# Optimization experiments

Measured on AMD Instinct MI355X. Metric: run time of the kernel, lower is better.

Reference implementation:

```python
import jax, jax.numpy as jnp
import numpy as np
from jax.scipy.special import logsumexp

B, S, T = 512, 512, 64


def setup_inputs() -> dict:
    key = jax.random.key(0)
    k1, k2, k3, k4, k5 = jax.random.split(key, 5)
    inputs = jax.random.normal(k1, (B, S, T), dtype=jnp.float32)
    tags = jax.random.randint(k2, (B, S), 0, T, dtype=jnp.int64)
    mask = jnp.ones((B, S), dtype=bool)
    # xavier_normal for (T, T): std = sqrt(2 / (T + T))
    transitions = jax.random.normal(k3, (T, T), dtype=jnp.float32) * np.sqrt(2.0 / (T + T))
    start_transitions = jax.random.normal(k4, (T,), dtype=jnp.float32)
    end_transitions = jax.random.normal(k5, (T,), dtype=jnp.float32)
    return {"inputs": inputs, "tags": tags, "mask": mask,
            "transitions": transitions,
            "start_transitions": start_transitions,
            "end_transitions": end_transitions}


def _input_likelihood(logits, mask, transitions, start_transitions, end_transitions):
    # logits: (B,S,T) -> time-major (S,B,T)
    logits_t = jnp.swapaxes(logits, 0, 1)
    mask_t = jnp.swapaxes(mask, 0, 1)
    alpha0 = start_transitions[None, :] + logits_t[0]  # (B,T)

    def step(alpha, xs):
        logit_i, m_i = xs  # (B,T), (B,)
        # inner[b, prev, cur] = alpha[b,prev] + logit_i[b,cur] + transitions[prev,cur]
        inner = alpha[:, :, None] + logit_i[:, None, :] + transitions[None, :, :]
        new_alpha = logsumexp(inner, axis=1)
        alpha = jnp.where(m_i[:, None], new_alpha, alpha)
        return alpha, None

    alpha, _ = jax.lax.scan(step, alpha0, (logits_t[1:], mask_t[1:]))
    stops = alpha + end_transitions[None, :]
    return logsumexp(stops, axis=-1)  # (B,)


def _joint_likelihood(logits, tags, mask, transitions, start_transitions, end_transitions):
    maskf = mask.astype(logits.dtype)  # (B,S)
    score = start_transitions[tags[:, 0]]  # (B,)
    # transition scores for steps 0..S-2 -> 1..S-1, masked by mask[:,1:]
    trans = transitions[tags[:, :-1], tags[:, 1:]] * maskf[:, 1:]
    # emission scores for steps 0..S-2, masked by mask[:,:-1]
    emit = jnp.take_along_axis(logits[:, :-1, :], tags[:, :-1, None], axis=2)[..., 0] * maskf[:, :-1]
    score = score + trans.sum(axis=1) + emit.sum(axis=1)
    last_idx = maskf.sum(axis=1).astype(jnp.int32) - 1
    last_tags = jnp.take_along_axis(tags, last_idx[:, None].astype(tags.dtype), axis=1)[:, 0]
    last_input_score = jnp.take_along_axis(logits[:, -1, :], last_tags[:, None], axis=1)[:, 0]
    score = score + end_transitions[last_tags] + last_input_score * maskf[:, -1]
    return score  # (B,)


def reference(inputs, tags, mask, transitions, start_transitions, end_transitions):
    log_denominator = _input_likelihood(inputs, mask, transitions, start_transitions, end_transitions)
    log_numerator = _joint_likelihood(inputs, tags, mask, transitions, start_transitions, end_transitions)
    return jnp.sum(log_numerator - log_denominator)
```

## Files before the change

kernel.cpp:

```cpp
#include <hip/hip_runtime.h>

#define CRF_B 512
#define CRF_S 512
#define CRF_T 64

__global__ __launch_bounds__(64, 1) void crf_fused_kernel(
    const float* __restrict__ logits,
    const int*   __restrict__ tags_raw,
    const float* __restrict__ trans,
    const float* __restrict__ start_t,
    const float* __restrict__ end_t,
    float* __restrict__ out)
{
    const int b = blockIdx.x;
    const int j = threadIdx.x;

    bool is64 = true;
    #pragma unroll
    for (int w = 1; w < 64; w += 2) is64 = is64 && (tags_raw[w] == 0);

    const float* lb = logits + (size_t)b * CRF_S * CRF_T;
    const int tbase = b * CRF_S;

    float num = 0.f;
    #pragma unroll
    for (int kk = 0; kk < CRF_S / 64; ++kk) {
        int i = kk * 64 + j;
        int ti = is64 ? tags_raw[(size_t)(tbase + i) * 2] : tags_raw[tbase + i];
        num += lb[i * CRF_T + ti];
        if (i == 0) {
            num += start_t[ti];
        } else {
            int tp = is64 ? tags_raw[(size_t)(tbase + i - 1) * 2]
                          : tags_raw[tbase + i - 1];
            num += trans[tp * CRF_T + ti];
        }
        if (i == CRF_S - 1) num += end_t[ti];
    }
    #pragma unroll
    for (int m = 32; m >= 1; m >>= 1) num += __shfl_xor(num, m, 64);

    float et[CRF_T];
    #pragma unroll
    for (int t = 0; t < CRF_T; ++t) et[t] = __expf(trans[t * CRF_T + j]);

    float a = __expf(start_t[j] + lb[j]);
    int K = 0;
    float elog = __expf(lb[CRF_T + j]);
    float lg_next = lb[2 * CRF_T + j];

    #pragma unroll 2
    for (int i = 1; i < CRF_S; ++i) {
        unsigned mbits = (unsigned)__builtin_amdgcn_readfirstlane(__float_as_int(a));
        int k = (int)(mbits >> 23) - 127;
        K += k;
        float scale = __int_as_float((unsigned)(127 - k) << 23);
        float mult = elog * scale;

        float acc0 = 0.f, acc1 = 0.f, acc2 = 0.f, acc3 = 0.f;
        int ai = __float_as_int(a);
        #pragma unroll
        for (int t = 0; t < CRF_T; t += 4) {
            acc0 = fmaf(__int_as_float(__builtin_amdgcn_readlane(ai, t + 0)), et[t + 0], acc0);
            acc1 = fmaf(__int_as_float(__builtin_amdgcn_readlane(ai, t + 1)), et[t + 1], acc1);
            acc2 = fmaf(__int_as_float(__builtin_amdgcn_readlane(ai, t + 2)), et[t + 2], acc2);
            acc3 = fmaf(__int_as_float(__builtin_amdgcn_readlane(ai, t + 3)), et[t + 3], acc3);
        }
        float s = (acc0 + acc1) + (acc2 + acc3);
        a = s * mult;

        elog = __expf(lg_next);
        int nxt = (i + 2 < CRF_S) ? (i + 2) : (CRF_S - 1);
        lg_next = lb[nxt * CRF_T + j];
    }

    float v = a * __expf(end_t[j]);
    #pragma unroll
    for (int m = 32; m >= 1; m >>= 1) v += __shfl_xor(v, m, 64);

    if (j == 0) {
        float logZ = __logf(v) + (float)K * 0.69314718055994531f;
        atomicAdd(out, num - logZ);
    }
}

extern "C" void kernel_launch(void* const* d_in, const int* in_sizes, int n_in,
                              void* d_out, int out_size, void* d_ws, size_t ws_size,
                              hipStream_t stream) {
    const float* logits  = (const float*)d_in[0];
    const int*   tags    = (const int*)d_in[1];
    const float* trans   = (const float*)d_in[3];
    const float* start_t = (const float*)d_in[4];
    const float* end_t   = (const float*)d_in[5];
    float* out = (float*)d_out;

    hipMemsetAsync(out, 0, sizeof(float) * (size_t)out_size, stream);
    crf_fused_kernel<<<dim3(CRF_B), dim3(64), 0, stream>>>(
        logits, tags, trans, start_t, end_t, out);
}
```

Measured before the change: 213.1 us.

## Broadcast alpha through LDS and use packed FMA for forward recursion

Replaces the 64 per-step readlane broadcasts of the alpha vector with one LDS store followed by float4 broadcast reads. The matvec now accumulates with v_pk_fma_f32 into eight packed accumulators. The aim is to remove the serialized scalar readlane path and halve the FMA instruction count. In exchange each step adds LDS store-to-load latency, relies on wave barriers for ordering, and drops the unroll-by-2 of the sequential loop.

```diff
diff --git a/kernel.cpp b/kernel.cpp
--- a/kernel.cpp
+++ b/kernel.cpp
@@ -3,6 +3,10 @@
 #define CRF_B 512
 #define CRF_S 512
 #define CRF_T 64
+
+typedef float v2f __attribute__((ext_vector_type(2)));
+
+#define PKFMA(acc, x, y) asm("v_pk_fma_f32 %0, %1, %2, %0" : "+v"(acc) : "v"(x), "v"(y))
 
 __global__ __launch_bounds__(64, 1) void crf_fused_kernel(
     const float* __restrict__ logits,
@@ -14,6 +18,8 @@
 {
     const int b = blockIdx.x;
     const int j = threadIdx.x;
+
+    __shared__ __align__(16) float a_lds[CRF_T];
 
     bool is64 = true;
     #pragma unroll
@@ -40,34 +46,50 @@
     #pragma unroll
     for (int m = 32; m >= 1; m >>= 1) num += __shfl_xor(num, m, 64);
 
-    float et[CRF_T];
+    v2f et2[CRF_T / 2];
     #pragma unroll
-    for (int t = 0; t < CRF_T; ++t) et[t] = __expf(trans[t * CRF_T + j]);
+    for (int t = 0; t < CRF_T; t += 2) {
+        et2[t / 2].x = __expf(trans[(t + 0) * CRF_T + j]);
+        et2[t / 2].y = __expf(trans[(t + 1) * CRF_T + j]);
+    }
 
     float a = __expf(start_t[j] + lb[j]);
     int K = 0;
     float elog = __expf(lb[CRF_T + j]);
     float lg_next = lb[2 * CRF_T + j];
 
-    #pragma unroll 2
     for (int i = 1; i < CRF_S; ++i) {
+        a_lds[j] = a;
+        __builtin_amdgcn_wave_barrier();
+
         unsigned mbits = (unsigned)__builtin_amdgcn_readfirstlane(__float_as_int(a));
         int k = (int)(mbits >> 23) - 127;
         K += k;
         float scale = __int_as_float((unsigned)(127 - k) << 23);
         float mult = elog * scale;
 
-        float acc0 = 0.f, acc1 = 0.f, acc2 = 0.f, acc3 = 0.f;
-        int ai = __float_as_int(a);
+        v2f p0 = {0.f, 0.f}, p1 = {0.f, 0.f}, p2 = {0.f, 0.f}, p3 = {0.f, 0.f};
+        v2f p4 = {0.f, 0.f}, p5 = {0.f, 0.f}, p6 = {0.f, 0.f}, p7 = {0.f, 0.f};
         #pragma unroll
-        for (int t = 0; t < CRF_T; t += 4) {
-            acc0 = fmaf(__int_as_float(__builtin_amdgcn_readlane(ai, t + 0)), et[t + 0], acc0);
-            acc1 = fmaf(__int_as_float(__builtin_amdgcn_readlane(ai, t + 1)), et[t + 1], acc1);
-            acc2 = fmaf(__int_as_float(__builtin_amdgcn_readlane(ai, t + 2)), et[t + 2], acc2);
-            acc3 = fmaf(__int_as_float(__builtin_amdgcn_readlane(ai, t + 3)), et[t + 3], acc3);
+        for (int t = 0; t < CRF_T; t += 16) {
+            float4 av0 = *(const float4*)&a_lds[t + 0];
+            float4 av1 = *(const float4*)&a_lds[t + 4];
+            float4 av2 = *(const float4*)&a_lds[t + 8];
+            float4 av3 = *(const float4*)&a_lds[t + 12];
+            v2f x;
+            x.x = av0.x; x.y = av0.y; PKFMA(p0, x, et2[(t >> 1) + 0]);
+            x.x = av0.z; x.y = av0.w; PKFMA(p1, x, et2[(t >> 1) + 1]);
+            x.x = av1.x; x.y = av1.y; PKFMA(p2, x, et2[(t >> 1) + 2]);
+            x.x = av1.z; x.y = av1.w; PKFMA(p3, x, et2[(t >> 1) + 3]);
+            x.x = av2.x; x.y = av2.y; PKFMA(p4, x, et2[(t >> 1) + 4]);
+            x.x = av2.z; x.y = av2.w; PKFMA(p5, x, et2[(t >> 1) + 5]);
+            x.x = av3.x; x.y = av3.y; PKFMA(p6, x, et2[(t >> 1) + 6]);
+            x.x = av3.z; x.y = av3.w; PKFMA(p7, x, et2[(t >> 1) + 7]);
         }
-        float s = (acc0 + acc1) + (acc2 + acc3);
-        a = s * mult;
+        __builtin_amdgcn_wave_barrier();
+
+        v2f r = ((p0 + p1) + (p2 + p3)) + ((p4 + p5) + (p6 + p7));
+        a = (r.x + r.y) * mult;
 
         elog = __expf(lg_next);
         int nxt = (i + 2 < CRF_S) ? (i + 2) : (CRF_S - 1);
```

Measured after the change: 294.8 us. 1.38x slower.

## Compute CRF forward recurrence with bf16 MFMA instead of readlane FMAs

Applied to the files above, without the earlier changes.

Replaces the per-step 64-element readlane/FMA dot product with bf16 MFMA 16x16x32 instructions. The exp(transitions) matrix is held in MFMA A fragments and the alpha vector is re-packed into B fragments each step. Rescaling moves to the exponent of the next step's emission, which is prefetched two steps ahead. This targets the serial readlane latency in the recurrence, at the cost of bf16 rounding of alpha and transitions that could exceed tolerance over 512 steps.

```diff
diff --git a/kernel.cpp b/kernel.cpp
--- a/kernel.cpp
+++ b/kernel.cpp
@@ -1,8 +1,21 @@
 #include <hip/hip_runtime.h>
+#include <hip/hip_bf16.h>
+#include <string.h>
 
 #define CRF_B 512
 #define CRF_S 512
 #define CRF_T 64
+#define LOG2E 1.4426950408889634f
+#define LN2   0.69314718055994531f
+
+typedef float  f32x4  __attribute__((ext_vector_type(4)));
+typedef short  bf16x8 __attribute__((ext_vector_type(8)));
+union Frag { bf16x8 f; unsigned d[4]; };
+
+__device__ __forceinline__ unsigned pack2(float lo, float hi) {
+    __hip_bfloat162 h2 = __float22bfloat162_rn(make_float2(lo, hi));
+    unsigned u; memcpy(&u, &h2, 4); return u;
+}
 
 __global__ __launch_bounds__(64, 1) void crf_fused_kernel(
     const float* __restrict__ logits,
@@ -12,20 +25,20 @@
     const float* __restrict__ end_t,
     float* __restrict__ out)
 {
-    const int b = blockIdx.x;
-    const int j = threadIdx.x;
+    const int b   = blockIdx.x;
+    const int L   = threadIdx.x;
+    const int Q   = L >> 4;
+    const int n16 = L & 15;
+    const float* lb = logits + (size_t)b * CRF_S * CRF_T;
 
     bool is64 = true;
     #pragma unroll
     for (int w = 1; w < 64; w += 2) is64 = is64 && (tags_raw[w] == 0);
-
-    const float* lb = logits + (size_t)b * CRF_S * CRF_T;
     const int tbase = b * CRF_S;
-
     float num = 0.f;
     #pragma unroll
     for (int kk = 0; kk < CRF_S / 64; ++kk) {
-        int i = kk * 64 + j;
+        int i = kk * 64 + L;
         int ti = is64 ? tags_raw[(size_t)(tbase + i) * 2] : tags_raw[tbase + i];
         num += lb[i * CRF_T + ti];
         if (i == 0) {
@@ -40,48 +53,103 @@
     #pragma unroll
     for (int m = 32; m >= 1; m >>= 1) num += __shfl_xor(num, m, 64);
 
-    float et[CRF_T];
+    Frag AF[4][2];
     #pragma unroll
-    for (int t = 0; t < CRF_T; ++t) et[t] = __expf(trans[t * CRF_T + j]);
+    for (int m = 0; m < 4; ++m)
+        #pragma unroll
+        for (int c = 0; c < 2; ++c) {
+            float v[8];
+            #pragma unroll
+            for (int u = 0; u < 8; ++u) {
+                int row = 16 * ((u >> 2) + 2 * c) + 4 * Q + (u & 3);
+                v[u] = __expf(trans[row * CRF_T + 16 * m + n16]);
+            }
+            #pragma unroll
+            for (int h = 0; h < 4; ++h)
+                AF[m][c].d[h] = pack2(v[2 * h], v[2 * h + 1]);
+        }
 
-    float a = __expf(start_t[j] + lb[j]);
-    int K = 0;
-    float elog = __expf(lb[CRF_T + j]);
-    float lg_next = lb[2 * CRF_T + j];
+    f32x4 a0[4];
+    #pragma unroll
+    for (int mm = 0; mm < 4; ++mm) {
+        f32x4 lg = *(const f32x4*)(lb + 16 * mm + 4 * Q);
+        f32x4 st = *(const f32x4*)(start_t + 16 * mm + 4 * Q);
+        #pragma unroll
+        for (int e = 0; e < 4; ++e) a0[mm][e] = __expf(st[e] + lg[e]);
+    }
+    Frag BF[2];
+    #pragma unroll
+    for (int c = 0; c < 2; ++c)
+        #pragma unroll
+        for (int h = 0; h < 4; ++h)
+            BF[c].d[h] = pack2(a0[2 * c + (h >> 1)][2 * (h & 1)],
+                               a0[2 * c + (h >> 1)][2 * (h & 1) + 1]);
 
+    float K = 0.f, kpend = 0.f;
+    f32x4 elsc[4], p1[4], p2[4];
+    #pragma unroll
+    for (int m = 0; m < 4; ++m) {
+        f32x4 lg1 = *(const f32x4*)(lb + 1 * CRF_T + 16 * m + 4 * Q);
+        #pragma unroll
+        for (int e = 0; e < 4; ++e) elsc[m][e] = exp2f(lg1[e] * LOG2E);
+        p1[m] = *(const f32x4*)(lb + 2 * CRF_T + 16 * m + 4 * Q);
+        p2[m] = *(const f32x4*)(lb + 3 * CRF_T + 16 * m + 4 * Q);
+    }
+
+    f32x4 w[4];
     #pragma unroll 2
     for (int i = 1; i < CRF_S; ++i) {
-        unsigned mbits = (unsigned)__builtin_amdgcn_readfirstlane(__float_as_int(a));
-        int k = (int)(mbits >> 23) - 127;
-        K += k;
-        float scale = __int_as_float((unsigned)(127 - k) << 23);
-        float mult = elog * scale;
+        K += kpend;
 
-        float acc0 = 0.f, acc1 = 0.f, acc2 = 0.f, acc3 = 0.f;
-        int ai = __float_as_int(a);
+        f32x4 acc[4];
         #pragma unroll
-        for (int t = 0; t < CRF_T; t += 4) {
-            acc0 = fmaf(__int_as_float(__builtin_amdgcn_readlane(ai, t + 0)), et[t + 0], acc0);
-            acc1 = fmaf(__int_as_float(__builtin_amdgcn_readlane(ai, t + 1)), et[t + 1], acc1);
-            acc2 = fmaf(__int_as_float(__builtin_amdgcn_readlane(ai, t + 2)), et[t + 2], acc2);
-            acc3 = fmaf(__int_as_float(__builtin_amdgcn_readlane(ai, t + 3)), et[t + 3], acc3);
+        for (int m = 0; m < 4; ++m) {
+            f32x4 z = {0.f, 0.f, 0.f, 0.f};
+            acc[m] = __builtin_amdgcn_mfma_f32_16x16x32_bf16(AF[m][0].f, BF[0].f, z, 0, 0, 0);
+            acc[m] = __builtin_amdgcn_mfma_f32_16x16x32_bf16(AF[m][1].f, BF[1].f, acc[m], 0, 0, 0);
         }
-        float s = (acc0 + acc1) + (acc2 + acc3);
-        a = s * mult;
 
-        elog = __expf(lg_next);
-        int nxt = (i + 2 < CRF_S) ? (i + 2) : (CRF_S - 1);
-        lg_next = lb[nxt * CRF_T + j];
+        unsigned bits = (unsigned)__builtin_amdgcn_readfirstlane(__float_as_int(acc[0].x));
+        float kf = (float)((int)(bits >> 23) - 127);
+        kpend = kf;
+
+        #pragma unroll
+        for (int m = 0; m < 4; ++m) w[m] = acc[m] * elsc[m];
+
+        BF[0].d[0] = pack2(w[0].x, w[0].y);
+        BF[0].d[1] = pack2(w[0].z, w[0].w);
+        BF[0].d[2] = pack2(w[1].x, w[1].y);
+        BF[0].d[3] = pack2(w[1].z, w[1].w);
+        BF[1].d[0] = pack2(w[2].x, w[2].y);
+        BF[1].d[1] = pack2(w[2].z, w[2].w);
+        BF[1].d[2] = pack2(w[3].x, w[3].y);
+        BF[1].d[3] = pack2(w[3].z, w[3].w);
+
+        #pragma unroll
+        for (int m = 0; m < 4; ++m) {
+            #pragma unroll
+            for (int e = 0; e < 4; ++e)
+                elsc[m][e] = exp2f(fmaf(p1[m][e], LOG2E, -kf));
+            p1[m] = p2[m];
+        }
+        int ip = (i + 3 < CRF_S) ? (i + 3) : (CRF_S - 1);
+        #pragma unroll
+        for (int m = 0; m < 4; ++m)
+            p2[m] = *(const f32x4*)(lb + (size_t)ip * CRF_T + 16 * m + 4 * Q);
     }
 
-    float v = a * __expf(end_t[j]);
+    float S = 0.f;
     #pragma unroll
-    for (int m = 32; m >= 1; m >>= 1) v += __shfl_xor(v, m, 64);
+    for (int m = 0; m < 4; ++m) {
+        f32x4 ed = *(const f32x4*)(end_t + 16 * m + 4 * Q);
+        #pragma unroll
+        for (int e = 0; e < 4; ++e) S += w[m][e] * __expf(ed[e]);
+    }
+    S += __shfl_xor(S, 16, 64);
+    S += __shfl_xor(S, 32, 64);
 
-    if (j == 0) {
-        float logZ = __logf(v) + (float)K * 0.69314718055994531f;
-        atomicAdd(out, num - logZ);
-    }
+    if (L == 0)
+        atomicAdd(out, num - (__logf(S) + K * LN2));
 }
 
 extern "C" void kernel_launch(void* const* d_in, const int* in_sizes, int n_in,
```

After: 468.6 us. +119.9%, slower.
